# Performance work log

Measured on AMD Instinct MI355X. Metric: run time of the kernel, lower is better.

## Reference

```python
import jax, jax.numpy as jnp
import numpy as np

B, S, A, FDIM, HDIM = 64, 4096, 128, 512, 512


def setup_inputs() -> dict:
    key = jax.random.key(0)
    k1, k2, k3, k4, k5 = jax.random.split(key, 5)
    return {
        "proj_image": jax.random.normal(k1, (B, S, A), dtype=jnp.float32),
        "image_features": jax.random.normal(k2, (B, S, FDIM), dtype=jnp.float32),
        "hidden_state": jax.random.normal(k3, (B, HDIM), dtype=jnp.float32),
        "W_hidden": jax.random.normal(k4, (A, HDIM), dtype=jnp.float32) / np.sqrt(HDIM),
        "w_score": jax.random.normal(k5, (A,), dtype=jnp.float32) / np.sqrt(A),
    }


def reference(proj_image, image_features, hidden_state, W_hidden, w_score):
    # proj_hidden: [B, A] = hidden_state @ W_hidden^T  (nn.Linear, no bias)
    proj_hidden = jnp.einsum("bh,ah->ba", hidden_state, W_hidden)
    # combined: [B, S, A] = tanh(proj_image + proj_hidden broadcast over S)
    combined = jnp.tanh(proj_image + proj_hidden[:, None, :])
    # scores: [B, S] = combined @ w_score (Linear dim->1, squeeze)
    scores = jnp.einsum("bsa,a->bs", combined, w_score)
    weights = jax.nn.softmax(scores, axis=-1)
    # context: [B, FDIM] = weights-weighted sum over S of image_features
    context = jnp.einsum("bs,bsd->bd", weights, image_features)
    return context, weights
```

## Files before the change

### kernel.cpp

```cpp
#include <hip/hip_runtime.h>

#define B_      64
#define S_      4096
#define A_      128
#define FDIM_   512
#define HDIM_   512
#define NCHUNK_ 32
#define SC_     (S_ / NCHUNK_)

__device__ __forceinline__ float fast_tanh(float x) {
    float e = __expf(2.0f * x);
    return (e - 1.0f) * __builtin_amdgcn_rcpf(e + 1.0f);
}

__global__ void k_proj_hidden(const float* __restrict__ hs,
                              const float* __restrict__ W,
                              float* __restrict__ ph) {
    int b = blockIdx.x;
    int a = threadIdx.x;
    __shared__ float s_h[HDIM_];
    for (int i = threadIdx.x; i < HDIM_; i += 128) s_h[i] = hs[b * HDIM_ + i];
    __syncthreads();
    const float4* Wr = (const float4*)(W + (size_t)a * HDIM_);
    const float4* Hr = (const float4*)s_h;
    float acc = 0.f;
#pragma unroll 8
    for (int h4 = 0; h4 < HDIM_ / 4; ++h4) {
        float4 w4 = Wr[h4];
        float4 h4v = Hr[h4];
        acc += w4.x * h4v.x + w4.y * h4v.y + w4.z * h4v.z + w4.w * h4v.w;
    }
    ph[b * A_ + a] = acc;
}

__global__ void k_scores(const float* __restrict__ proj,
                         const float* __restrict__ ph,
                         const float* __restrict__ wsc,
                         float* __restrict__ scores) {
    int tid = threadIdx.x;
    int sub = tid & 31;
    int row = (blockIdx.x << 3) | (tid >> 5);
    int b = row >> 12;
    float4 p = ((const float4*)(proj + (size_t)row * A_))[sub];
    float4 h = ((const float4*)(ph + b * A_))[sub];
    float4 w = ((const float4*)wsc)[sub];
    float v = fast_tanh(p.x + h.x) * w.x
            + fast_tanh(p.y + h.y) * w.y
            + fast_tanh(p.z + h.z) * w.z
            + fast_tanh(p.w + h.w) * w.w;
#pragma unroll
    for (int m = 16; m; m >>= 1) v += __shfl_xor(v, m, 64);
    if (sub == 0) scores[row] = v;
}

__global__ void k_softmax(const float* __restrict__ scores,
                          float* __restrict__ weights) {
    int b = blockIdx.x;
    int tid = threadIdx.x;
    int lane = tid & 63, wv = tid >> 6;
    __shared__ float s_red[16];

    float4 v = ((const float4*)(scores + (size_t)b * S_))[tid];

    float mx = fmaxf(fmaxf(v.x, v.y), fmaxf(v.z, v.w));
#pragma unroll
    for (int m = 32; m; m >>= 1) mx = fmaxf(mx, __shfl_xor(mx, m, 64));
    if (lane == 0) s_red[wv] = mx;
    __syncthreads();
    mx = s_red[0];
#pragma unroll
    for (int i = 1; i < 16; ++i) mx = fmaxf(mx, s_red[i]);
    __syncthreads();

    float4 e;
    e.x = __expf(v.x - mx); e.y = __expf(v.y - mx);
    e.z = __expf(v.z - mx); e.w = __expf(v.w - mx);
    float sum = e.x + e.y + e.z + e.w;
#pragma unroll
    for (int m = 32; m; m >>= 1) sum += __shfl_xor(sum, m, 64);
    if (lane == 0) s_red[wv] = sum;
    __syncthreads();
    sum = 0.f;
#pragma unroll
    for (int i = 0; i < 16; ++i) sum += s_red[i];
    float inv = __builtin_amdgcn_rcpf(sum);

    float4 o = {e.x * inv, e.y * inv, e.z * inv, e.w * inv};
    ((float4*)(weights + (size_t)b * S_))[tid] = o;
}

__global__ void k_context_part(const float* __restrict__ feat,
                               const float* __restrict__ weights,
                               float* __restrict__ part) {
    int b = blockIdx.y;
    int c = blockIdx.x;
    int tid = threadIdx.x;
    int d4 = (tid & 127) << 2;
    int sg = tid >> 7;
    int s0 = c * SC_;

    const float* wrow = weights + (size_t)b * S_ + s0;
    const float* fbase = feat + ((size_t)b * S_ + s0) * FDIM_ + d4;

    float4 acc = {0.f, 0.f, 0.f, 0.f};
#pragma unroll 4
    for (int i = sg; i < SC_; i += 2) {
        float w = wrow[i];
        float4 f = *(const float4*)(fbase + (size_t)i * FDIM_);
        acc.x += w * f.x;
        acc.y += w * f.y;
        acc.z += w * f.z;
        acc.w += w * f.w;
    }

    __shared__ float4 s_acc[128];
    if (sg == 1) s_acc[tid & 127] = acc;
    __syncthreads();
    if (sg == 0) {
        float4 o = s_acc[tid];
        o.x += acc.x; o.y += acc.y; o.z += acc.z; o.w += acc.w;
        *(float4*)(part + ((size_t)(b * NCHUNK_ + c)) * FDIM_ + d4) = o;
    }
}

__global__ void k_context_reduce(const float* __restrict__ part,
                                 float* __restrict__ ctx) {
    int b = blockIdx.x;
    int tid = threadIdx.x;
    int d4 = tid << 2;
    float4 acc = {0.f, 0.f, 0.f, 0.f};
#pragma unroll
    for (int c = 0; c < NCHUNK_; ++c) {
        float4 p = *(const float4*)(part + ((size_t)(b * NCHUNK_ + c)) * FDIM_ + d4);
        acc.x += p.x; acc.y += p.y; acc.z += p.z; acc.w += p.w;
    }
    *(float4*)(ctx + (size_t)b * FDIM_ + d4) = acc;
}

extern "C" void kernel_launch(void* const* d_in, const int* in_sizes, int n_in,
                              void* d_out, int out_size, void* d_ws, size_t ws_size,
                              hipStream_t stream) {
    const float* proj_image     = (const float*)d_in[0];
    const float* image_features = (const float*)d_in[1];
    const float* hidden_state   = (const float*)d_in[2];
    const float* W_hidden       = (const float*)d_in[3];
    const float* w_score        = (const float*)d_in[4];

    float* out     = (float*)d_out;
    float* ctx     = out;
    float* weights = out + B_ * FDIM_;

    float* ph     = (float*)d_ws;
    float* scores = ph + B_ * A_;
    float* part   = scores + (size_t)B_ * S_;

    k_proj_hidden<<<B_, 128, 0, stream>>>(hidden_state, W_hidden, ph);
    k_scores<<<(B_ * S_) / 8, 256, 0, stream>>>(proj_image, ph, w_score, scores);
    k_softmax<<<B_, 1024, 0, stream>>>(scores, weights);
    dim3 gctx(NCHUNK_, B_);
    k_context_part<<<gctx, 256, 0, stream>>>(image_features, weights, part);
    k_context_reduce<<<B_, 128, 0, stream>>>(part, ctx);
}
```

Measured before the change: 761.4 us.

## Replace partial-sum reduce kernel with atomics and reuse output buffers as scratch

Drops the separate context-reduce kernel: each chunk block now atomically adds its partial context into the zero-initialised output, with a memset inserted first. Scores are written straight into the weights output and softmax runs in place, and proj_hidden is stored in the ctx region before that region is cleared. The chunk count falls from 32 to 8, giving 512 blocks that each stream longer runs of features. The aim is to cut one launch and the partial-buffer traffic, at the cost of fewer blocks for the memory-bound pass and some atomic contention.

```diff
diff --git a/kernel.cpp b/kernel.cpp
--- a/kernel.cpp
+++ b/kernel.cpp
@@ -5,7 +5,7 @@
 #define A_      128
 #define FDIM_   512
 #define HDIM_   512
-#define NCHUNK_ 32
+#define NCHUNK_ 8
 #define SC_     (S_ / NCHUNK_)
 
 __device__ __forceinline__ float fast_tanh(float x) {
@@ -53,14 +53,13 @@
     if (sub == 0) scores[row] = v;
 }
 
-__global__ void k_softmax(const float* __restrict__ scores,
-                          float* __restrict__ weights) {
+__global__ void k_softmax(float* __restrict__ buf) {
     int b = blockIdx.x;
     int tid = threadIdx.x;
     int lane = tid & 63, wv = tid >> 6;
     __shared__ float s_red[16];
 
-    float4 v = ((const float4*)(scores + (size_t)b * S_))[tid];
+    float4 v = ((const float4*)(buf + (size_t)b * S_))[tid];
 
     float mx = fmaxf(fmaxf(v.x, v.y), fmaxf(v.z, v.w));
 #pragma unroll
@@ -86,12 +85,12 @@
     float inv = __builtin_amdgcn_rcpf(sum);
 
     float4 o = {e.x * inv, e.y * inv, e.z * inv, e.w * inv};
-    ((float4*)(weights + (size_t)b * S_))[tid] = o;
+    ((float4*)(buf + (size_t)b * S_))[tid] = o;
 }
 
-__global__ void k_context_part(const float* __restrict__ feat,
-                               const float* __restrict__ weights,
-                               float* __restrict__ part) {
+__global__ void k_context(const float* __restrict__ feat,
+                          const float* __restrict__ weights,
+                          float* __restrict__ ctx) {
     int b = blockIdx.y;
     int c = blockIdx.x;
     int tid = threadIdx.x;
@@ -118,23 +117,12 @@
     __syncthreads();
     if (sg == 0) {
         float4 o = s_acc[tid];
-        o.x += acc.x; o.y += acc.y; o.z += acc.z; o.w += acc.w;
-        *(float4*)(part + ((size_t)(b * NCHUNK_ + c)) * FDIM_ + d4) = o;
+        float* p = ctx + (size_t)b * FDIM_ + d4;
+        atomicAdd(p + 0, o.x + acc.x);
+        atomicAdd(p + 1, o.y + acc.y);
+        atomicAdd(p + 2, o.z + acc.z);
+        atomicAdd(p + 3, o.w + acc.w);
     }
-}
-
-__global__ void k_context_reduce(const float* __restrict__ part,
-                                 float* __restrict__ ctx) {
-    int b = blockIdx.x;
-    int tid = threadIdx.x;
-    int d4 = tid << 2;
-    float4 acc = {0.f, 0.f, 0.f, 0.f};
-#pragma unroll
-    for (int c = 0; c < NCHUNK_; ++c) {
-        float4 p = *(const float4*)(part + ((size_t)(b * NCHUNK_ + c)) * FDIM_ + d4);
-        acc.x += p.x; acc.y += p.y; acc.z += p.z; acc.w += p.w;
-    }
-    *(float4*)(ctx + (size_t)b * FDIM_ + d4) = acc;
 }
 
 extern "C" void kernel_launch(void* const* d_in, const int* in_sizes, int n_in,
@@ -150,14 +138,12 @@
     float* ctx     = out;
     float* weights = out + B_ * FDIM_;
 
-    float* ph     = (float*)d_ws;
-    float* scores = ph + B_ * A_;
-    float* part   = scores + (size_t)B_ * S_;
+    float* ph = ctx;
 
     k_proj_hidden<<<B_, 128, 0, stream>>>(hidden_state, W_hidden, ph);
-    k_scores<<<(B_ * S_) / 8, 256, 0, stream>>>(proj_image, ph, w_score, scores);
-    k_softmax<<<B_, 1024, 0, stream>>>(scores, weights);
+    k_scores<<<(B_ * S_) / 8, 256, 0, stream>>>(proj_image, ph, w_score, weights);
+    k_softmax<<<B_, 1024, 0, stream>>>(weights);
+    hipMemsetAsync(ctx, 0, (size_t)B_ * FDIM_ * sizeof(float), stream);
     dim3 gctx(NCHUNK_, B_);
-    k_context_part<<<gctx, 256, 0, stream>>>(image_features, weights, part);
-    k_context_reduce<<<B_, 128, 0, stream>>>(part, ctx);
+    k_context<<<gctx, 256, 0, stream>>>(image_features, weights, ctx);
 }
```

Measured after the change: 757.1 us. No clear change (-0.6%).
